# Kernel tuning notes

Measured on AMD Instinct MI355X. Metric: run time of the kernel, lower is better.

The kernel has to match this reference:

```python
import jax, jax.numpy as jnp
import numpy as np

DT_SCALE = 0.01  # time grid = arange(T) * 0.01, i.e. t in [0, 0.99]


def setup_inputs() -> dict:
    key = jax.random.key(0)
    k1, k2, k3 = jax.random.split(key, 3)
    latents, hidden = 128, 256
    S, N, T = 4, 1024, 100
    first_point = jax.random.normal(k1, (S, N, latents), dtype=jnp.float32)
    time_steps_to_predict = jnp.arange(T, dtype=jnp.float32) * DT_SCALE
    # ODEFunc MLP params (Glorot-ish scaling so tanh stays in a sane range)
    W1 = jax.random.normal(k2, (latents, hidden), dtype=jnp.float32) / np.sqrt(latents)
    b1 = jnp.zeros((hidden,), dtype=jnp.float32)
    W2 = jax.random.normal(k3, (hidden, latents), dtype=jnp.float32) / np.sqrt(hidden)
    b2 = jnp.zeros((latents,), dtype=jnp.float32)
    return {
        "first_point": first_point,
        "time_steps_to_predict": time_steps_to_predict,
        "W1": W1, "b1": b1, "W2": W2, "b2": b2,
    }


def reference(first_point, time_steps_to_predict, W1, b1, W2, b2):
    # ode_func: dy/dt = tanh(y @ W1 + b1) @ W2 + b2 (time-autonomous MLP)
    def f(y):
        return jnp.tanh(y @ W1 + b1) @ W2 + b2

    # torchdiffeq fixed-step 'rk4': one classical RK4 step per output interval.
    t0s = time_steps_to_predict[:-1]
    t1s = time_steps_to_predict[1:]

    def rk4_step(y, ts):
        t0, t1 = ts
        dt = t1 - t0
        half = dt * 0.5
        k1 = f(y)
        k2 = f(y + half * k1)
        k3 = f(y + half * k2)
        k4 = f(y + dt * k3)
        y1 = y + (dt / 6.0) * (k1 + 2.0 * k2 + 2.0 * k3 + k4)
        return y1, y1

    _, ys = jax.lax.scan(rk4_step, first_point, (t0s, t1s))  # [T-1, S, N, D]
    pred_y = jnp.concatenate([first_point[None], ys], axis=0)  # [T, S, N, D]
    # permute(1, 2, 0, 3): [T, S, N, D] -> [S, N, T, D]
    return jnp.transpose(pred_y, (1, 2, 0, 3))
```

## Files before the change

kernel.cpp:

```cpp
#include <hip/hip_runtime.h>
#include <hip/hip_bf16.h>

typedef __attribute__((ext_vector_type(8))) short v8s;
typedef __attribute__((ext_vector_type(8))) unsigned short u8s;
typedef __attribute__((ext_vector_type(4))) float f4;

#define MFMA16(a, b, c) __builtin_amdgcn_mfma_f32_16x16x32_bf16((a), (b), (c), 0, 0, 0)

__device__ __forceinline__ float bf2f(unsigned short u) {
    return __uint_as_float(((unsigned)u) << 16);
}
__device__ __forceinline__ unsigned short f2bf(float x) {
    unsigned u = __float_as_uint(x);
    unsigned r = 0x7FFFu + ((u >> 16) & 1u);
    return (unsigned short)((u + r) >> 16);
}
__device__ __forceinline__ unsigned pack_bf16_2(float a, float b) {
    float2 t; t.x = a; t.y = b;
    union { __hip_bfloat162 h; unsigned u; } cv;
    cv.h = __float22bfloat162_rn(t);
    return cv.u;
}
__device__ __forceinline__ float tanh_scaled(float zs) {
    float u = __builtin_amdgcn_exp2f(zs);
    float r = __builtin_amdgcn_rcpf(u + 1.0f);
    return __builtin_fmaf(-2.0f, r, 1.0f);
}
__device__ __forceinline__ float ldin(const void* p, int i, bool f32) {
    return f32 ? ((const float*)p)[i] : bf2f(((const unsigned short*)p)[i]);
}

#define BROWS 16
#define TSTEPS 100
#define DLAT 128
#define DHID 256
#define HSTR 256
#define HBUF (BROWS * HSTR)
#define TANH_C 2.885390081777927f

__global__ __launch_bounds__(256, 4)
void prep_w21(const void* __restrict__ ts, const void* __restrict__ W1,
              const void* __restrict__ W2, const void* __restrict__ b2,
              void* __restrict__ ws) {
    const bool m32 = fabsf(((const float*)ts)[1] - 0.01f) < 0.004f;
    const int i = blockIdx.x;
    const int j = threadIdx.x;
    float acc = 0.f;
    for (int m = 0; m < DLAT; ++m)
        acc = __builtin_fmaf(ldin(W2, i * DLAT + m, m32), ldin(W1, m * DHID + j, m32), acc);
    ((unsigned short*)ws)[i * DHID + j] = f2bf(TANH_C * acc);
    if (i == 0) {
        float a2 = 0.f;
        for (int m = 0; m < DLAT; ++m)
            a2 = __builtin_fmaf(ldin(b2, m, m32), ldin(W1, m * DHID + j, m32), a2);
        ((float*)((char*)ws + DHID * DHID * 2))[j] = TANH_C * a2;
    }
}

__global__ __launch_bounds__(512, 2)
void ode_rk4_kernel(const void* __restrict__ fp,
                    const void* __restrict__ ts,
                    const void* __restrict__ W1,
                    const void* __restrict__ b1,
                    const void* __restrict__ W2,
                    const void* __restrict__ b2,
                    const void* __restrict__ ws,
                    void* __restrict__ out) {
    __shared__ unsigned short hB[2 * HBUF];
    __shared__ float tsL[TSTEPS];

    const bool m32 = fabsf(((const float*)ts)[1] - 0.01f) < 0.004f;

    const int tid = threadIdx.x;
    const int w = tid >> 6;
    const int lane = tid & 63;
    const int pp = lane & 15;
    const int qq = lane >> 4;
    const int R0 = blockIdx.x * BROWS;

    if (tid < TSTEPS) tsL[tid] = ldin(ts, tid, m32);

    const unsigned short* w21p = (const unsigned short*)ws;
    v8s w21f[8][2];
#pragma unroll
    for (int kt = 0; kt < 8; ++kt)
#pragma unroll
        for (int nt = 0; nt < 2; ++nt) {
            v8s f;
#pragma unroll
            for (int j = 0; j < 8; ++j)
                f[j] = (short)w21p[(kt * 32 + qq * 8 + j) * DHID + 32 * w + nt * 16 + pp];
            w21f[kt][nt] = f;
        }
    v8s w2f[8];
#pragma unroll
    for (int kt = 0; kt < 8; ++kt) {
        v8s f;
#pragma unroll
        for (int j = 0; j < 8; ++j)
            f[j] = (short)f2bf(ldin(W2, (kt * 32 + qq * 8 + j) * DLAT + 16 * w + pp, m32));
        w2f[kt] = f;
    }
    const float* b2w1p = (const float*)((const char*)ws + DHID * DHID * 2);
    float bz[2];
#pragma unroll
    for (int nt = 0; nt < 2; ++nt) bz[nt] = b2w1p[32 * w + 16 * nt + pp];
    const float b2v = ldin(b2, 16 * w + pp, m32);

    const int spp = (pp & 7) ^ ((pp & 8) >> 2);
    int hAoff[8];
#pragma unroll
    for (int kt = 0; kt < 8; ++kt)
        hAoff[kt] = pp * HSTR + (((4 * kt + qq) ^ spp) << 3);
    const int pb = pp >> 3, pw = pp & 7;
    int hoffs[2][4];
#pragma unroll
    for (int nt = 0; nt < 2; ++nt)
#pragma unroll
        for (int r = 0; r < 4; ++r) {
            int row = 4 * qq + r;
            int s = (row & 7) ^ ((row & 8) >> 2);
            hoffs[nt][r] = row * HSTR + (((4 * w + 2 * nt + pb) ^ s) << 3) + pw;
        }

    if (m32) {
        int row = tid >> 5, ch = tid & 31;
        int s = (row & 7) ^ ((row & 8) >> 2);
        float4 v = *((const float4*)((const float*)fp + (size_t)(R0 + row) * DLAT) + ch);
        *((float4*)((float*)out + ((size_t)(R0 + row) * TSTEPS) * DLAT) + ch) = v;
        ushort4 b; b.x = f2bf(v.x); b.y = f2bf(v.y); b.z = f2bf(v.z); b.w = f2bf(v.w);
        *(ushort4*)(hB + row * HSTR + (((ch >> 1) ^ s) << 3) + (ch & 1) * 4) = b;
    } else if (tid < 256) {
        int row = tid >> 4, ch = tid & 15;
        int s = (row & 7) ^ ((row & 8) >> 2);
        const unsigned short* fpu = (const unsigned short*)fp;
        u8s v = *((const u8s*)(fpu + (size_t)(R0 + row) * DLAT) + ch);
        *((u8s*)((unsigned short*)out + ((size_t)(R0 + row) * TSTEPS) * DLAT) + ch) = v;
        *(u8s*)(hB + row * HSTR + ((ch ^ s) << 3)) = v;
    }

    float yreg[4];
    int ob[4];
#pragma unroll
    for (int r = 0; r < 4; ++r) {
        yreg[r] = ldin(fp, (R0 + 4 * qq + r) * DLAT + 16 * w + pp, m32);
        ob[r] = (R0 + 4 * qq + r) * (TSTEPS * DLAT) + 16 * w + pp;
    }

    v8s w1f[4][2];
#pragma unroll
    for (int kt = 0; kt < 4; ++kt)
#pragma unroll
        for (int nt = 0; nt < 2; ++nt) {
            v8s f;
#pragma unroll
            for (int j = 0; j < 8; ++j)
                f[j] = (short)f2bf(TANH_C * ldin(W1, (kt * 32 + qq * 8 + j) * DHID + 32 * w + nt * 16 + pp, m32));
            w1f[kt][nt] = f;
        }
    float b1s[2];
#pragma unroll
    for (int nt = 0; nt < 2; ++nt) b1s[nt] = TANH_C * ldin(b1, 32 * w + 16 * nt + pp, m32);

    __syncthreads();
    float zs[8];
    {
        v8s a0[4];
#pragma unroll
        for (int kt = 0; kt < 4; ++kt) a0[kt] = *(const v8s*)(hB + hAoff[kt]);
#pragma unroll
        for (int nt = 0; nt < 2; ++nt) {
            f4 az = {0.f, 0.f, 0.f, 0.f};
#pragma unroll
            for (int kt = 0; kt < 4; ++kt) az = MFMA16(a0[kt], w1f[kt][nt], az);
            float th[4];
#pragma unroll
            for (int r = 0; r < 4; ++r) {
                zs[nt * 4 + r] = az[r] + b1s[nt];
                th[r] = tanh_scaled(zs[nt * 4 + r]);
            }
            unsigned short* wp = hB + HBUF;
            unsigned p0 = pack_bf16_2(th[0], th[1]);
            unsigned p1 = pack_bf16_2(th[2], th[3]);
            wp[hoffs[nt][0]] = (unsigned short)p0;
            wp[hoffs[nt][1]] = (unsigned short)(p0 >> 16);
            wp[hoffs[nt][2]] = (unsigned short)p1;
            wp[hoffs[nt][3]] = (unsigned short)(p1 >> 16);
        }
    }

    v8s a[2][8];
    float ksum[4] = {0.f, 0.f, 0.f, 0.f};
    float d6p = 0.f;

    for (int t = 0; t < TSTEPS - 1; ++t) {
        const float dt = tsL[t + 1] - tsL[t];
        const float half = 0.5f * dt;
        const float d6 = dt * (1.0f / 6.0f);
        float zsum[8] = {0.f, 0.f, 0.f, 0.f, 0.f, 0.f, 0.f, 0.f};
#pragma unroll
        for (int e = 0; e < 4; ++e) {
            const int rb = (e & 1) ^ 1;
            const int wb = e & 1;
            __syncthreads();
            const unsigned short* hbase = hB + rb * HBUF;
            unsigned short* wbase = hB + wb * HBUF;
#pragma unroll
            for (int kt = 0; kt < 8; ++kt) a[wb][kt] = *(const v8s*)(hbase + hAoff[kt]);

            const bool hasPrev = (e > 0) || (t > 0);
            if (hasPrev) {
                const float wgtP = (e >= 2) ? 2.0f : 1.0f;
                f4 ak = {0.f, 0.f, 0.f, 0.f};
#pragma unroll
                for (int kt = 0; kt < 8; ++kt) ak = MFMA16(a[wb ^ 1][kt], w2f[kt], ak);
#pragma unroll
                for (int r = 0; r < 4; ++r)
                    ksum[r] = __builtin_fmaf(wgtP, ak[r] + b2v, ksum[r]);
                if (e == 0) {
#pragma unroll
                    for (int r = 0; r < 4; ++r)
                        yreg[r] = __builtin_fmaf(d6p, ksum[r], yreg[r]);
                    if (m32) {
                        float* op = (float*)out;
#pragma unroll
                        for (int r = 0; r < 4; ++r) op[ob[r] + t * DLAT] = yreg[r];
                    } else {
                        unsigned short* op = (unsigned short*)out;
#pragma unroll
                        for (int r = 0; r < 4; ++r) op[ob[r] + t * DLAT] = f2bf(yreg[r]);
                    }
#pragma unroll
                    for (int r = 0; r < 4; ++r) ksum[r] = 0.f;
                }
            }

            const float wgt = (e == 0 || e == 3) ? 1.0f : 2.0f;
            const float cc = (e == 2) ? dt : half;
#pragma unroll
            for (int nt = 0; nt < 2; ++nt) {
                f4 az = {0.f, 0.f, 0.f, 0.f};
#pragma unroll
                for (int kt = 0; kt < 8; ++kt) az = MFMA16(a[wb][kt], w21f[kt][nt], az);
                float th[4];
#pragma unroll
                for (int r = 0; r < 4; ++r) {
                    float kz = az[r] + bz[nt];
                    zsum[nt * 4 + r] = __builtin_fmaf(wgt, kz, zsum[nt * 4 + r]);
                    float ztv;
                    if (e < 3) {
                        ztv = __builtin_fmaf(cc, kz, zs[nt * 4 + r]);
                    } else {
                        zs[nt * 4 + r] = __builtin_fmaf(d6, zsum[nt * 4 + r], zs[nt * 4 + r]);
                        ztv = zs[nt * 4 + r];
                    }
                    th[r] = tanh_scaled(ztv);
                }
                unsigned p0 = pack_bf16_2(th[0], th[1]);
                unsigned p1 = pack_bf16_2(th[2], th[3]);
                wbase[hoffs[nt][0]] = (unsigned short)p0;
                wbase[hoffs[nt][1]] = (unsigned short)(p0 >> 16);
                wbase[hoffs[nt][2]] = (unsigned short)p1;
                wbase[hoffs[nt][3]] = (unsigned short)(p1 >> 16);
            }
        }
        d6p = d6;
    }

    {
        f4 ak = {0.f, 0.f, 0.f, 0.f};
#pragma unroll
        for (int kt = 0; kt < 8; ++kt) ak = MFMA16(a[1][kt], w2f[kt], ak);
#pragma unroll
        for (int r = 0; r < 4; ++r) {
            ksum[r] += ak[r] + b2v;
            yreg[r] = __builtin_fmaf(d6p, ksum[r], yreg[r]);
        }
        if (m32) {
            float* op = (float*)out;
#pragma unroll
            for (int r = 0; r < 4; ++r) op[ob[r] + (TSTEPS - 1) * DLAT] = yreg[r];
        } else {
            unsigned short* op = (unsigned short*)out;
#pragma unroll
            for (int r = 0; r < 4; ++r) op[ob[r] + (TSTEPS - 1) * DLAT] = f2bf(yreg[r]);
        }
    }
}

extern "C" void kernel_launch(void* const* d_in, const int* in_sizes, int n_in,
                              void* d_out, int out_size, void* d_ws, size_t ws_size,
                              hipStream_t stream) {
    (void)in_sizes; (void)n_in; (void)out_size; (void)ws_size;
    prep_w21<<<DHID, DHID, 0, stream>>>(d_in[1], d_in[2], d_in[4], d_in[5], d_ws);
    ode_rk4_kernel<<<256, 512, 0, stream>>>(d_in[0], d_in[1], d_in[2], d_in[3],
                                            d_in[4], d_in[5], d_ws, d_out);
}
```

Baseline: 527.1 us.

## Accumulate weighted RK4 tanh activations and apply W2 once per step

```diff
diff --git a/kernel.cpp b/kernel.cpp
--- a/kernel.cpp
+++ b/kernel.cpp
@@ -6,6 +6,11 @@
 typedef __attribute__((ext_vector_type(4))) float f4;
 
 #define MFMA16(a, b, c) __builtin_amdgcn_mfma_f32_16x16x32_bf16((a), (b), (c), 0, 0, 0)
+
+#define LBAR() do { \
+    asm volatile("s_waitcnt lgkmcnt(0)\n\ts_barrier" ::: "memory"); \
+    __builtin_amdgcn_sched_barrier(0); \
+} while (0)
 
 __device__ __forceinline__ float bf2f(unsigned short u) {
     return __uint_as_float(((unsigned)u) << 16);
@@ -67,6 +72,7 @@
                     const void* __restrict__ ws,
                     void* __restrict__ out) {
     __shared__ unsigned short hB[2 * HBUF];
+    __shared__ unsigned short pB[HBUF];
     __shared__ float tsL[TSTEPS];
 
     const bool m32 = fabsf(((const float*)ts)[1] - 0.01f) < 0.004f;
@@ -164,6 +170,7 @@
 
     __syncthreads();
     float zs[8];
+    float pacc[8];
     {
         v8s a0[4];
 #pragma unroll
@@ -178,6 +185,7 @@
             for (int r = 0; r < 4; ++r) {
                 zs[nt * 4 + r] = az[r] + b1s[nt];
                 th[r] = tanh_scaled(zs[nt * 4 + r]);
+                pacc[nt * 4 + r] = th[r];
             }
             unsigned short* wp = hB + HBUF;
             unsigned p0 = pack_bf16_2(th[0], th[1]);
@@ -189,9 +197,8 @@
         }
     }
 
-    v8s a[2][8];
-    float ksum[4] = {0.f, 0.f, 0.f, 0.f};
-    float d6p = 0.f;
+    v8s pf[8];
+    float d6p = 0.f, dtp = 0.f;
 
     for (int t = 0; t < TSTEPS - 1; ++t) {
         const float dt = tsL[t + 1] - tsL[t];
@@ -202,46 +209,44 @@
         for (int e = 0; e < 4; ++e) {
             const int rb = (e & 1) ^ 1;
             const int wb = e & 1;
-            __syncthreads();
+            LBAR();
             const unsigned short* hbase = hB + rb * HBUF;
             unsigned short* wbase = hB + wb * HBUF;
-#pragma unroll
-            for (int kt = 0; kt < 8; ++kt) a[wb][kt] = *(const v8s*)(hbase + hAoff[kt]);
-
-            const bool hasPrev = (e > 0) || (t > 0);
-            if (hasPrev) {
-                const float wgtP = (e >= 2) ? 2.0f : 1.0f;
-                f4 ak = {0.f, 0.f, 0.f, 0.f};
-#pragma unroll
-                for (int kt = 0; kt < 8; ++kt) ak = MFMA16(a[wb ^ 1][kt], w2f[kt], ak);
-#pragma unroll
-                for (int r = 0; r < 4; ++r)
-                    ksum[r] = __builtin_fmaf(wgtP, ak[r] + b2v, ksum[r]);
-                if (e == 0) {
-#pragma unroll
-                    for (int r = 0; r < 4; ++r)
-                        yreg[r] = __builtin_fmaf(d6p, ksum[r], yreg[r]);
-                    if (m32) {
-                        float* op = (float*)out;
-#pragma unroll
-                        for (int r = 0; r < 4; ++r) op[ob[r] + t * DLAT] = yreg[r];
-                    } else {
-                        unsigned short* op = (unsigned short*)out;
-#pragma unroll
-                        for (int r = 0; r < 4; ++r) op[ob[r] + t * DLAT] = f2bf(yreg[r]);
-                    }
-#pragma unroll
-                    for (int r = 0; r < 4; ++r) ksum[r] = 0.f;
+            v8s a[8];
+#pragma unroll
+            for (int kt = 0; kt < 8; ++kt) a[kt] = *(const v8s*)(hbase + hAoff[kt]);
+            if (e == 3) {
+#pragma unroll
+                for (int kt = 0; kt < 8; ++kt) pf[kt] = *(const v8s*)(pB + hAoff[kt]);
+            }
+            if (e == 0 && t > 0) {
+                f4 kp = {0.f, 0.f, 0.f, 0.f};
+#pragma unroll
+                for (int kt = 0; kt < 8; ++kt) kp = MFMA16(pf[kt], w2f[kt], kp);
+#pragma unroll
+                for (int r = 0; r < 4; ++r) {
+                    float t0 = __builtin_fmaf(dtp, b2v, yreg[r]);
+                    yreg[r] = __builtin_fmaf(d6p, kp[r], t0);
+                }
+                if (m32) {
+                    float* op = (float*)out;
+#pragma unroll
+                    for (int r = 0; r < 4; ++r) op[ob[r] + t * DLAT] = yreg[r];
+                } else {
+                    unsigned short* op = (unsigned short*)out;
+#pragma unroll
+                    for (int r = 0; r < 4; ++r) op[ob[r] + t * DLAT] = f2bf(yreg[r]);
                 }
             }
 
             const float wgt = (e == 0 || e == 3) ? 1.0f : 2.0f;
             const float cc = (e == 2) ? dt : half;
+            const float wP = (e == 0 || e == 1) ? 2.0f : 1.0f;
 #pragma unroll
             for (int nt = 0; nt < 2; ++nt) {
                 f4 az = {0.f, 0.f, 0.f, 0.f};
 #pragma unroll
-                for (int kt = 0; kt < 8; ++kt) az = MFMA16(a[wb][kt], w21f[kt][nt], az);
+                for (int kt = 0; kt < 8; ++kt) az = MFMA16(a[kt], w21f[kt][nt], az);
                 float th[4];
 #pragma unroll
                 for (int r = 0; r < 4; ++r) {
@@ -255,6 +260,8 @@
                         ztv = zs[nt * 4 + r];
                     }
                     th[r] = tanh_scaled(ztv);
+                    if (e == 3) pacc[nt * 4 + r] = th[r];
+                    else pacc[nt * 4 + r] = __builtin_fmaf(wP, th[r], pacc[nt * 4 + r]);
                 }
                 unsigned p0 = pack_bf16_2(th[0], th[1]);
                 unsigned p1 = pack_bf16_2(th[2], th[3]);
@@ -262,19 +269,27 @@
                 wbase[hoffs[nt][1]] = (unsigned short)(p0 >> 16);
                 wbase[hoffs[nt][2]] = (unsigned short)p1;
                 wbase[hoffs[nt][3]] = (unsigned short)(p1 >> 16);
+                if (e == 2) {
+                    unsigned q0 = pack_bf16_2(pacc[nt * 4 + 0], pacc[nt * 4 + 1]);
+                    unsigned q1 = pack_bf16_2(pacc[nt * 4 + 2], pacc[nt * 4 + 3]);
+                    pB[hoffs[nt][0]] = (unsigned short)q0;
+                    pB[hoffs[nt][1]] = (unsigned short)(q0 >> 16);
+                    pB[hoffs[nt][2]] = (unsigned short)q1;
+                    pB[hoffs[nt][3]] = (unsigned short)(q1 >> 16);
+                }
             }
         }
-        d6p = d6;
+        d6p = d6; dtp = dt;
     }
 
     {
-        f4 ak = {0.f, 0.f, 0.f, 0.f};
-#pragma unroll
-        for (int kt = 0; kt < 8; ++kt) ak = MFMA16(a[1][kt], w2f[kt], ak);
+        f4 kp = {0.f, 0.f, 0.f, 0.f};
+#pragma unroll
+        for (int kt = 0; kt < 8; ++kt) kp = MFMA16(pf[kt], w2f[kt], kp);
 #pragma unroll
         for (int r = 0; r < 4; ++r) {
-            ksum[r] += ak[r] + b2v;
-            yreg[r] = __builtin_fmaf(d6p, ksum[r], yreg[r]);
+            float t0 = __builtin_fmaf(dtp, b2v, yreg[r]);
+            yreg[r] = __builtin_fmaf(d6p, kp[r], t0);
         }
         if (m32) {
             float* op = (float*)out;
```

Result: no change. 522.1 us (-1.0%).
